# Kernel tuning notes

Hardware: AMD Instinct MI355X
Metric: run time of the kernel (lower is better)

## Reference

```python
import jax, jax.numpy as jnp
import numpy as np

N = 6144      # nodes
NFEAT = 512
NHID = 256
NHEADS = 4
DHEAD = NHID // NHEADS  # 64
NEMBED = 128
NEG_INF = -9e15
LRELU_ALPHA = 0.2


def setup_inputs() -> dict:
    key = jax.random.key(0)
    k = jax.random.split(key, 8)
    x = jax.random.normal(k[0], (N, NFEAT), dtype=jnp.float32)
    adj = (jax.random.uniform(k[1], (N, N)) < 0.01).astype(jnp.int32)
    # per-head GAT params, packed over heads
    W = jax.random.normal(k[2], (NHEADS, NFEAT, DHEAD), dtype=jnp.float32) * 0.05
    a_src = jax.random.normal(k[3], (NHEADS, DHEAD), dtype=jnp.float32) * 0.05
    a_dst = jax.random.normal(k[4], (NHEADS, DHEAD), dtype=jnp.float32) * 0.05
    # output linear (init.normal_ std=0.05 per reset_parameters)
    lin_w = jax.random.normal(k[5], (NEMBED, NHID), dtype=jnp.float32) * 0.05
    lin_b = jnp.zeros((NEMBED,), dtype=jnp.float32)
    return {"x": x, "adj": adj, "W": W, "a_src": a_src, "a_dst": a_dst,
            "lin_w": lin_w, "lin_b": lin_b}


def _gat_forward(x, adj, W, a_src, a_dst, lin_w, lin_b):
    # Wh: [H, N, D]
    Wh = jnp.einsum('nf,hfd->hnd', x, W)
    # attention logits e_ij = leakyrelu(a_src.Wh_i + a_dst.Wh_j): [H, N, N]
    s = jnp.einsum('hnd,hd->hn', Wh, a_src)   # source term per node
    t = jnp.einsum('hnd,hd->hn', Wh, a_dst)   # target term per node
    e = s[:, :, None] + t[:, None, :]
    e = jax.nn.leaky_relu(e, negative_slope=LRELU_ALPHA)
    # mask by adjacency, softmax over neighbors
    e = jnp.where(adj[None, :, :] > 0, e, NEG_INF)
    attn = jax.nn.softmax(e, axis=-1)
    # aggregate and per-head ELU (concat=True GAT layer)
    h = jnp.einsum('hnm,hmd->hnd', attn, Wh)
    h = jax.nn.elu(h)
    # concat heads -> [N, NHID]
    h = jnp.transpose(h, (1, 0, 2)).reshape(N, NHID)
    # dropout is identity in eval mode; linear + ELU
    out = jax.nn.elu(h @ lin_w.T + lin_b)
    return out


def reference(x, adj, W, a_src, a_dst, lin_w, lin_b):
    return _gat_forward(x, adj, W, a_src, a_dst, lin_w, lin_b)
```

## Files before the change

### kernel.cpp

```cpp
#include <hip/hip_runtime.h>
#include <hip/hip_bf16.h>
#include <math.h>

#define N_NODES 6144
#define NFEAT 512
#define NHID 256
#define NHEADS 4
#define DHEAD 64
#define NEMBED 128
#define LRELU_ALPHA 0.2f
#define MAXC 256
#define ASTRIDE 20

__global__ __launch_bounds__(256) void gemm_scan(const float* __restrict__ x,
                                                 const float* __restrict__ W,
                                                 const float* __restrict__ a_src,
                                                 const float* __restrict__ a_dst,
                                                 const int* __restrict__ adj,
                                                 float* __restrict__ Wh,
                                                 float* __restrict__ s_arr,
                                                 float* __restrict__ t_arr,
                                                 int* __restrict__ cnt_g,
                                                 unsigned short* __restrict__ nbr_g) {
    __shared__ float As[64][ASTRIDE];
    __shared__ float Bs[16][64];
    const int tid = threadIdx.x;

    if (blockIdx.y < NHEADS) {
        const int tx = tid & 15;
        const int ty = tid >> 4;
        const int row0 = blockIdx.x * 64;
        const int h = blockIdx.y;
        const float* Bp = W + (size_t)h * NFEAT * DHEAD;

        float acc[4][4] = {};

        for (int k0 = 0; k0 < NFEAT; k0 += 16) {
            {
                const int r = tid >> 2, kq = tid & 3;
                const float4 v = *(const float4*)(x + (size_t)(row0 + r) * NFEAT + k0 + kq * 4);
                *(float4*)&As[r][kq * 4] = v;
            }
            {
                const int kk = tid >> 4, cq = tid & 15;
                const float4 v = *(const float4*)(Bp + (size_t)(k0 + kk) * DHEAD + cq * 4);
                *(float4*)&Bs[kk][cq * 4] = v;
            }
            __syncthreads();
#pragma unroll
            for (int kk = 0; kk < 16; kk++) {
                float a[4], b[4];
#pragma unroll
                for (int i = 0; i < 4; i++) a[i] = As[ty * 4 + i][kk];
#pragma unroll
                for (int j = 0; j < 4; j++) b[j] = Bs[kk][tx * 4 + j];
#pragma unroll
                for (int i = 0; i < 4; i++)
#pragma unroll
                    for (int j = 0; j < 4; j++) acc[i][j] += a[i] * b[j];
            }
            __syncthreads();
        }
#pragma unroll
        for (int i = 0; i < 4; i++) {
            const int row = row0 + ty * 4 + i;
            float4 v = make_float4(acc[i][0], acc[i][1], acc[i][2], acc[i][3]);
            *(float4*)(Wh + ((size_t)h * N_NODES + row) * DHEAD + tx * 4) = v;
        }
        float a4s[4], a4d[4];
#pragma unroll
        for (int j = 0; j < 4; j++) {
            a4s[j] = a_src[h * DHEAD + tx * 4 + j];
            a4d[j] = a_dst[h * DHEAD + tx * 4 + j];
        }
#pragma unroll
        for (int i = 0; i < 4; i++) {
            float ps = acc[i][0] * a4s[0] + acc[i][1] * a4s[1] +
                       acc[i][2] * a4s[2] + acc[i][3] * a4s[3];
            float pt = acc[i][0] * a4d[0] + acc[i][1] * a4d[1] +
                       acc[i][2] * a4d[2] + acc[i][3] * a4d[3];
#pragma unroll
            for (int off = 1; off < 16; off <<= 1) {
                ps += __shfl_xor(ps, off);
                pt += __shfl_xor(pt, off);
            }
            if (tx == 0) {
                const int row = row0 + ty * 4 + i;
                s_arr[h * N_NODES + row] = ps;
                t_arr[h * N_NODES + row] = pt;
            }
        }
    } else {
        const int r = (blockIdx.y - NHEADS) * gridDim.x + blockIdx.x;
        const int* arow = adj + (size_t)r * N_NODES;
        unsigned short* nrow = nbr_g + (size_t)r * MAXC;
        int* cp = cnt_g + r;
#pragma unroll
        for (int it = 0; it < 6; ++it) {
            const int j0 = it * 1024 + tid * 4;
            const int4 v = *(const int4*)(arow + j0);
            const int n = (v.x != 0) + (v.y != 0) + (v.z != 0) + (v.w != 0);
            if (n) {
                int base = atomicAdd(cp, n);
                if (v.x) { if (base < MAXC) nrow[base] = (unsigned short)j0; ++base; }
                if (v.y) { if (base < MAXC) nrow[base] = (unsigned short)(j0 + 1); ++base; }
                if (v.z) { if (base < MAXC) nrow[base] = (unsigned short)(j0 + 2); ++base; }
                if (v.w) { if (base < MAXC) nrow[base] = (unsigned short)(j0 + 3); }
            }
        }
    }
}

__global__ __launch_bounds__(256) void attn_agg(const int* __restrict__ adj,
                                                const float* __restrict__ Wh,
                                                const float* __restrict__ s_arr,
                                                const float* __restrict__ t_arr,
                                                const int* __restrict__ cnt_g,
                                                const unsigned short* __restrict__ nbr_g,
                                                float* __restrict__ hcat) {
    __shared__ unsigned short nbr[MAXC];
    __shared__ float p_s[NHEADS][MAXC];
    const int i = blockIdx.x;
    const int tid = threadIdx.x;
    const int h = tid >> 6;
    const int lane = tid & 63;
    const int c = cnt_g[i];
    const float* whp = Wh + (size_t)h * N_NODES * DHEAD;

    float acc, l;
    if (c > 0 && c <= MAXC) {
        for (int k = tid; k < c; k += 256) nbr[k] = nbr_g[(size_t)i * MAXC + k];
        __syncthreads();

        const float s_h = s_arr[h * N_NODES + i];
        const float* tp = t_arr + (size_t)h * N_NODES;
        float m = -INFINITY;
        for (int k = lane; k < c; k += 64) {
            float e = s_h + tp[nbr[k]];
            e = e >= 0.0f ? e : LRELU_ALPHA * e;
            p_s[h][k] = e;
            m = fmaxf(m, e);
        }
#pragma unroll
        for (int off = 32; off > 0; off >>= 1) m = fmaxf(m, __shfl_xor(m, off));
        float ls = 0.0f;
        for (int k = lane; k < c; k += 64) {
            const float p = __expf(p_s[h][k] - m);
            p_s[h][k] = p;
            ls += p;
        }
#pragma unroll
        for (int off = 32; off > 0; off >>= 1) ls += __shfl_xor(ls, off);
        l = ls;

        float a0 = 0.f, a1 = 0.f, a2 = 0.f, a3 = 0.f;
        float a4 = 0.f, a5 = 0.f, a6 = 0.f, a7 = 0.f;
        int k = 0;
        for (; k + 8 <= c; k += 8) {
            const int j0 = nbr[k],     j1 = nbr[k + 1], j2 = nbr[k + 2], j3 = nbr[k + 3];
            const int j4 = nbr[k + 4], j5 = nbr[k + 5], j6 = nbr[k + 6], j7 = nbr[k + 7];
            const float p0 = p_s[h][k],     p1 = p_s[h][k + 1];
            const float p2 = p_s[h][k + 2], p3 = p_s[h][k + 3];
            const float p4 = p_s[h][k + 4], p5 = p_s[h][k + 5];
            const float p6 = p_s[h][k + 6], p7 = p_s[h][k + 7];
            a0 += p0 * whp[(size_t)j0 * DHEAD + lane];
            a1 += p1 * whp[(size_t)j1 * DHEAD + lane];
            a2 += p2 * whp[(size_t)j2 * DHEAD + lane];
            a3 += p3 * whp[(size_t)j3 * DHEAD + lane];
            a4 += p4 * whp[(size_t)j4 * DHEAD + lane];
            a5 += p5 * whp[(size_t)j5 * DHEAD + lane];
            a6 += p6 * whp[(size_t)j6 * DHEAD + lane];
            a7 += p7 * whp[(size_t)j7 * DHEAD + lane];
        }
        for (; k < c; k++) a0 += p_s[h][k] * whp[(size_t)nbr[k] * DHEAD + lane];
        acc = ((a0 + a1) + (a2 + a3)) + ((a4 + a5) + (a6 + a7));
    } else if (c == 0) {
        acc = 0.0f;
        for (int j = 0; j < N_NODES; j++) acc += whp[(size_t)j * DHEAD + lane];
        l = (float)N_NODES;
    } else {
        const int* arow = adj + (size_t)i * N_NODES;
        const float s_h = s_arr[h * N_NODES + i];
        const float* tp = t_arr + (size_t)h * N_NODES;
        float m = -INFINITY, ll = 0.0f;
        acc = 0.0f;
        for (int j = 0; j < N_NODES; j++) {
            if (arow[j]) {
                float e = s_h + tp[j];
                e = e >= 0.0f ? e : LRELU_ALPHA * e;
                const float m_new = fmaxf(m, e);
                const float scale = __expf(m - m_new);
                const float p = __expf(e - m_new);
                ll = ll * scale + p;
                acc = acc * scale + p * whp[(size_t)j * DHEAD + lane];
                m = m_new;
            }
        }
        l = ll;
    }
    float hv = acc / l;
    hv = hv > 0.0f ? hv : expm1f(hv);
    hcat[(size_t)i * NHID + h * DHEAD + lane] = hv;
}

__global__ __launch_bounds__(256) void out_gemm(const float* __restrict__ hcat,
                                                const float* __restrict__ lin_w,
                                                const float* __restrict__ lin_b,
                                                float* __restrict__ out) {
    __shared__ float As[64][ASTRIDE * 4];
    __shared__ float Bs[16][64];
    const int tid = threadIdx.x;
    const int tx = tid & 15;
    const int ty = tid >> 4;
    const int row0 = blockIdx.x * 64;
    const int c0 = blockIdx.y * 64;

    float acc[4][4] = {};

    for (int k0 = 0; k0 < NHID; k0 += 16) {
        {
            const int r = tid >> 2, kq = tid & 3;
            const float4 v = *(const float4*)(hcat + (size_t)(row0 + r) * NHID + k0 + kq * 4);
            *(float4*)&As[r][kq * 4] = v;
        }
        {
            const int cc = tid & 63, kq = tid >> 6;
            const float4 v = *(const float4*)(lin_w + (size_t)(c0 + cc) * NHID + k0 + kq * 4);
            Bs[kq * 4 + 0][cc] = v.x;
            Bs[kq * 4 + 1][cc] = v.y;
            Bs[kq * 4 + 2][cc] = v.z;
            Bs[kq * 4 + 3][cc] = v.w;
        }
        __syncthreads();
#pragma unroll
        for (int kk = 0; kk < 16; kk++) {
            float a[4], b[4];
#pragma unroll
            for (int i = 0; i < 4; i++) a[i] = As[ty * 4 + i][kk];
#pragma unroll
            for (int j = 0; j < 4; j++) b[j] = Bs[kk][tx * 4 + j];
#pragma unroll
            for (int i = 0; i < 4; i++)
#pragma unroll
                for (int j = 0; j < 4; j++) acc[i][j] += a[i] * b[j];
        }
        __syncthreads();
    }
#pragma unroll
    for (int i = 0; i < 4; i++) {
        const int row = row0 + ty * 4 + i;
        float v[4];
#pragma unroll
        for (int j = 0; j < 4; j++) {
            const int col = c0 + tx * 4 + j;
            float val = acc[i][j] + lin_b[col];
            v[j] = val > 0.0f ? val : expm1f(val);
        }
        *(float4*)(out + (size_t)row * NEMBED + c0 + tx * 4) =
            make_float4(v[0], v[1], v[2], v[3]);
    }
}

extern "C" void kernel_launch(void* const* d_in, const int* in_sizes, int n_in,
                              void* d_out, int out_size, void* d_ws, size_t ws_size,
                              hipStream_t stream) {
    const float* x     = (const float*)d_in[0];
    const int*   adj   = (const int*)d_in[1];
    const float* W     = (const float*)d_in[2];
    const float* a_src = (const float*)d_in[3];
    const float* a_dst = (const float*)d_in[4];
    const float* lin_w = (const float*)d_in[5];
    const float* lin_b = (const float*)d_in[6];
    float* out = (float*)d_out;

    float* Wh   = (float*)d_ws;
    float* s    = Wh + (size_t)NHEADS * N_NODES * DHEAD;
    float* t    = s + (size_t)NHEADS * N_NODES;
    float* hcat = t + (size_t)NHEADS * N_NODES;
    int* cnt_g  = (int*)(hcat + (size_t)N_NODES * NHID);
    unsigned short* nbr_g = (unsigned short*)(cnt_g + N_NODES);

    hipMemsetAsync(cnt_g, 0, N_NODES * sizeof(int), stream);
    gemm_scan<<<dim3(96, NHEADS + 64), 256, 0, stream>>>(
        x, W, a_src, a_dst, adj, Wh, s, t, cnt_g, nbr_g);
    attn_agg<<<N_NODES, 256, 0, stream>>>(adj, Wh, s, t, cnt_g, nbr_g, hcat);
    out_gemm<<<dim3(N_NODES / 64, NEMBED / 64), 256, 0, stream>>>(hcat, lin_w, lin_b, out);
}
```

Before: 286.5 us.

## Store Wh as bf16 and gather two neighbors per wave in aggregation

The projected features Wh are now written in bf16 instead of fp32, which halves the bytes gathered per neighbor in the attention aggregation. Each wave splits into two halves that handle alternating neighbors. Each lane loads a packed pair of bf16 features, and the two halves are combined with a cross-half shuffle at the end. This cuts gather traffic and load instructions at the cost of bf16 rounding error in Wh, and the fp32 s/t logits are kept. Small writes of 8 bytes per thread in the GEMM epilogue are also reduced.

```diff
diff --git a/kernel.cpp b/kernel.cpp
--- a/kernel.cpp
+++ b/kernel.cpp
@@ -12,12 +12,18 @@
 #define MAXC 256
 #define ASTRIDE 20
 
+static __device__ __forceinline__ unsigned short f2bf(float f) {
+    unsigned u = __float_as_uint(f);
+    unsigned r = (u + 0x7FFFu + ((u >> 16) & 1u)) >> 16;
+    return (unsigned short)r;
+}
+
 __global__ __launch_bounds__(256) void gemm_scan(const float* __restrict__ x,
                                                  const float* __restrict__ W,
                                                  const float* __restrict__ a_src,
                                                  const float* __restrict__ a_dst,
                                                  const int* __restrict__ adj,
-                                                 float* __restrict__ Wh,
+                                                 unsigned short* __restrict__ Whb,
                                                  float* __restrict__ s_arr,
                                                  float* __restrict__ t_arr,
                                                  int* __restrict__ cnt_g,
@@ -64,8 +70,12 @@
 #pragma unroll
         for (int i = 0; i < 4; i++) {
             const int row = row0 + ty * 4 + i;
-            float4 v = make_float4(acc[i][0], acc[i][1], acc[i][2], acc[i][3]);
-            *(float4*)(Wh + ((size_t)h * N_NODES + row) * DHEAD + tx * 4) = v;
+            ushort4 w;
+            w.x = f2bf(acc[i][0]);
+            w.y = f2bf(acc[i][1]);
+            w.z = f2bf(acc[i][2]);
+            w.w = f2bf(acc[i][3]);
+            *(ushort4*)(Whb + ((size_t)h * N_NODES + row) * DHEAD + tx * 4) = w;
         }
         float a4s[4], a4d[4];
 #pragma unroll
@@ -112,7 +122,7 @@
 }
 
 __global__ __launch_bounds__(256) void attn_agg(const int* __restrict__ adj,
-                                                const float* __restrict__ Wh,
+                                                const unsigned short* __restrict__ Whb,
                                                 const float* __restrict__ s_arr,
                                                 const float* __restrict__ t_arr,
                                                 const int* __restrict__ cnt_g,
@@ -124,10 +134,13 @@
     const int tid = threadIdx.x;
     const int h = tid >> 6;
     const int lane = tid & 63;
+    const int half = lane >> 5;
+    const int dp = (lane & 31) * 2;
     const int c = cnt_g[i];
-    const float* whp = Wh + (size_t)h * N_NODES * DHEAD;
-
-    float acc, l;
+    const unsigned short* wp = Whb + (size_t)h * N_NODES * DHEAD;
+
+    float r0 = 0.0f, r1 = 0.0f, l = 1.0f;
+    bool combine = true;
     if (c > 0 && c <= MAXC) {
         for (int k = tid; k < c; k += 256) nbr[k] = nbr_g[(size_t)i * MAXC + k];
         __syncthreads();
@@ -153,37 +166,44 @@
         for (int off = 32; off > 0; off >>= 1) ls += __shfl_xor(ls, off);
         l = ls;
 
-        float a0 = 0.f, a1 = 0.f, a2 = 0.f, a3 = 0.f;
-        float a4 = 0.f, a5 = 0.f, a6 = 0.f, a7 = 0.f;
+        float ax[8] = {0.f, 0.f, 0.f, 0.f, 0.f, 0.f, 0.f, 0.f};
+        float ay[8] = {0.f, 0.f, 0.f, 0.f, 0.f, 0.f, 0.f, 0.f};
         int k = 0;
-        for (; k + 8 <= c; k += 8) {
-            const int j0 = nbr[k],     j1 = nbr[k + 1], j2 = nbr[k + 2], j3 = nbr[k + 3];
-            const int j4 = nbr[k + 4], j5 = nbr[k + 5], j6 = nbr[k + 6], j7 = nbr[k + 7];
-            const float p0 = p_s[h][k],     p1 = p_s[h][k + 1];
-            const float p2 = p_s[h][k + 2], p3 = p_s[h][k + 3];
-            const float p4 = p_s[h][k + 4], p5 = p_s[h][k + 5];
-            const float p6 = p_s[h][k + 6], p7 = p_s[h][k + 7];
-            a0 += p0 * whp[(size_t)j0 * DHEAD + lane];
-            a1 += p1 * whp[(size_t)j1 * DHEAD + lane];
-            a2 += p2 * whp[(size_t)j2 * DHEAD + lane];
-            a3 += p3 * whp[(size_t)j3 * DHEAD + lane];
-            a4 += p4 * whp[(size_t)j4 * DHEAD + lane];
-            a5 += p5 * whp[(size_t)j5 * DHEAD + lane];
-            a6 += p6 * whp[(size_t)j6 * DHEAD + lane];
-            a7 += p7 * whp[(size_t)j7 * DHEAD + lane];
-        }
-        for (; k < c; k++) a0 += p_s[h][k] * whp[(size_t)nbr[k] * DHEAD + lane];
-        acc = ((a0 + a1) + (a2 + a3)) + ((a4 + a5) + (a6 + a7));
+        for (; k + 16 <= c; k += 16) {
+#pragma unroll
+            for (int s2 = 0; s2 < 8; ++s2) {
+                const int kk = k + 2 * s2 + half;
+                const int j = nbr[kk];
+                const float p = p_s[h][kk];
+                const unsigned w = *(const unsigned*)(wp + (size_t)j * DHEAD + dp);
+                ax[s2] += p * __uint_as_float(w << 16);
+                ay[s2] += p * __uint_as_float(w & 0xffff0000u);
+            }
+        }
+        for (; k < c; k += 2) {
+            const int kk = k + half;
+            int j = nbr[k];
+            float p = 0.0f;
+            if (kk < c) { j = nbr[kk]; p = p_s[h][kk]; }
+            const unsigned w = *(const unsigned*)(wp + (size_t)j * DHEAD + dp);
+            ax[0] += p * __uint_as_float(w << 16);
+            ay[0] += p * __uint_as_float(w & 0xffff0000u);
+        }
+        r0 = ((ax[0] + ax[1]) + (ax[2] + ax[3])) + ((ax[4] + ax[5]) + (ax[6] + ax[7]));
+        r1 = ((ay[0] + ay[1]) + (ay[2] + ay[3])) + ((ay[4] + ay[5]) + (ay[6] + ay[7]));
     } else if (c == 0) {
-        acc = 0.0f;
-        for (int j = 0; j < N_NODES; j++) acc += whp[(size_t)j * DHEAD + lane];
+        for (int j = half; j < N_NODES; j += 2) {
+            const unsigned w = *(const unsigned*)(wp + (size_t)j * DHEAD + dp);
+            r0 += __uint_as_float(w << 16);
+            r1 += __uint_as_float(w & 0xffff0000u);
+        }
         l = (float)N_NODES;
     } else {
+        combine = false;
         const int* arow = adj + (size_t)i * N_NODES;
         const float s_h = s_arr[h * N_NODES + i];
         const float* tp = t_arr + (size_t)h * N_NODES;
         float m = -INFINITY, ll = 0.0f;
-        acc = 0.0f;
         for (int j = 0; j < N_NODES; j++) {
             if (arow[j]) {
                 float e = s_h + tp[j];
@@ -192,15 +212,24 @@
                 const float scale = __expf(m - m_new);
                 const float p = __expf(e - m_new);
                 ll = ll * scale + p;
-                acc = acc * scale + p * whp[(size_t)j * DHEAD + lane];
+                const unsigned w = *(const unsigned*)(wp + (size_t)j * DHEAD + dp);
+                r0 = r0 * scale + p * __uint_as_float(w << 16);
+                r1 = r1 * scale + p * __uint_as_float(w & 0xffff0000u);
                 m = m_new;
             }
         }
         l = ll;
     }
-    float hv = acc / l;
-    hv = hv > 0.0f ? hv : expm1f(hv);
-    hcat[(size_t)i * NHID + h * DHEAD + lane] = hv;
+    if (combine) {
+        r0 += __shfl_xor(r0, 32);
+        r1 += __shfl_xor(r1, 32);
+    }
+    float hx = r0 / l, hy = r1 / l;
+    hx = hx > 0.0f ? hx : expm1f(hx);
+    hy = hy > 0.0f ? hy : expm1f(hy);
+    if (lane < 32) {
+        *(float2*)(hcat + (size_t)i * NHID + h * DHEAD + dp) = make_float2(hx, hy);
+    }
 }
 
 __global__ __launch_bounds__(256) void out_gemm(const float* __restrict__ hcat,
@@ -273,8 +302,8 @@
     const float* lin_b = (const float*)d_in[6];
     float* out = (float*)d_out;
 
-    float* Wh   = (float*)d_ws;
-    float* s    = Wh + (size_t)NHEADS * N_NODES * DHEAD;
+    unsigned short* Whb = (unsigned short*)d_ws;
+    float* s    = (float*)(Whb + (size_t)NHEADS * N_NODES * DHEAD);
     float* t    = s + (size_t)NHEADS * N_NODES;
     float* hcat = t + (size_t)NHEADS * N_NODES;
     int* cnt_g  = (int*)(hcat + (size_t)N_NODES * NHID);
@@ -282,7 +311,7 @@
 
     hipMemsetAsync(cnt_g, 0, N_NODES * sizeof(int), stream);
     gemm_scan<<<dim3(96, NHEADS + 64), 256, 0, stream>>>(
-        x, W, a_src, a_dst, adj, Wh, s, t, cnt_g, nbr_g);
-    attn_agg<<<N_NODES, 256, 0, stream>>>(adj, Wh, s, t, cnt_g, nbr_g, hcat);
+        x, W, a_src, a_dst, adj, Whb, s, t, cnt_g, nbr_g);
+    attn_agg<<<N_NODES, 256, 0, stream>>>(adj, Whb, s, t, cnt_g, nbr_g, hcat);
     out_gemm<<<dim3(N_NODES / 64, NEMBED / 64), 256, 0, stream>>>(hcat, lin_w, lin_b, out);
 }
```

Result: faster. 277.9 us (-3.0%).
